# Kernel optimization log

Hardware: AMD Instinct MI355X
Metric: run time of the kernel (lower is better)

## Reference

```python
import jax, jax.numpy as jnp
import numpy as np

TEMP = 0.07
W_MLM, W_LINE, W_QUAT, W_SONNET = 0.5, 0.2, 0.2, 0.1
IGNORE = -100


def setup_inputs() -> dict:
    key = jax.random.key(0)
    ks = jax.random.split(key, 10)
    B, S, V, D = 16, 256, 30522, 768
    P_LINE, N_LINE = 224, 224
    P_QUAT, N_QUAT = 64, 64
    mlm_logits = jax.random.normal(ks[0], (B, S, V), dtype=jnp.float32)
    raw_labels = jax.random.randint(ks[1], (B, S), 0, V)
    mask_prob = jax.random.uniform(ks[2], (B, S))
    mlm_labels = jnp.where(mask_prob < 0.15, raw_labels, IGNORE).astype(jnp.int64)
    return {
        "mlm_logits": mlm_logits,
        "mlm_labels": mlm_labels,
        "line_anchor": jax.random.normal(ks[3], (P_LINE, D), dtype=jnp.float32),
        "line_positive": jax.random.normal(ks[4], (P_LINE, D), dtype=jnp.float32),
        "line_negative": jax.random.normal(ks[5], (N_LINE, D), dtype=jnp.float32),
        "quat_anchor": jax.random.normal(ks[6], (P_QUAT, D), dtype=jnp.float32),
        "quat_positive": jax.random.normal(ks[7], (P_QUAT, D), dtype=jnp.float32),
        "quat_negative": jax.random.normal(ks[8], (N_QUAT, D), dtype=jnp.float32),
        "sonnet_embeddings": jax.random.normal(ks[9], (B, D), dtype=jnp.float32),
    }


def _l2norm(x, eps=1e-12):
    # matches F.normalize(dim=-1)
    n = jnp.sqrt(jnp.sum(x * x, axis=-1, keepdims=True))
    return x / jnp.maximum(n, eps)


def _mlm_loss(logits, labels):
    # cross entropy with ignore_index=-100, mean over valid tokens
    V = logits.shape[-1]
    logits2 = logits.reshape(-1, V)
    labels1 = labels.reshape(-1)
    valid = labels1 != IGNORE
    safe = jnp.where(valid, labels1, 0)
    logp = jax.nn.log_softmax(logits2, axis=-1)
    nll = -jnp.take_along_axis(logp, safe[:, None], axis=-1)[:, 0]
    nll = jnp.where(valid, nll, 0.0)
    return jnp.sum(nll) / jnp.maximum(jnp.sum(valid), 1)


def _infonce(anchor, positive, negatives):
    # batched form of the python-loop pairwise InfoNCE:
    # each anchor scored against its positive and ALL negatives
    a = _l2norm(anchor)                       # [P, D]
    p = _l2norm(positive)                     # [P, D]
    n = _l2norm(negatives)                    # [N, D]
    pos_sim = jnp.sum(a * p, axis=-1) / TEMP  # [P]
    neg_sim = jnp.einsum("pd,nd->pn", a, n) / TEMP  # [P, N]
    logits = jnp.concatenate([pos_sim[:, None], neg_sim], axis=1)  # [P, 1+N]
    loss = jax.nn.logsumexp(logits, axis=1) - pos_sim
    return jnp.mean(loss)


def _sonnet_loss(emb):
    sn = _l2norm(emb)                                  # [B, D]
    sim = jnp.einsum("id,jd->ij", sn, sn) / TEMP       # [B, B]
    diag = jnp.diagonal(sim)
    loss = jax.nn.logsumexp(sim, axis=1) - diag
    return jnp.mean(loss)


def reference(mlm_logits, mlm_labels, line_anchor, line_positive, line_negative,
              quat_anchor, quat_positive, quat_negative, sonnet_embeddings):
    mlm = _mlm_loss(mlm_logits, mlm_labels)
    line = _infonce(line_anchor, line_positive, line_negative)
    quat = _infonce(quat_anchor, quat_positive, quat_negative)
    sonnet = _sonnet_loss(sonnet_embeddings)
    total = W_MLM * mlm + W_LINE * line + W_QUAT * quat + W_SONNET * sonnet
    return total
```

## Files before the change

### kernel.cpp

```cpp
#include <hip/hip_runtime.h>
#include <math.h>
#include <stdint.h>

#define TI (1.0f / 0.07f)
#define VD 768
#define VD4 192
#define VV 30522
#define NROWS 4096
#define P_LINE 224
#define N_LINE 224
#define P_QUAT 64
#define N_QUAT 64

#define WS_NLL   0
#define WS_FLAG  4096
#define WS_LINE  8192
#define WS_QUAT  8416

__device__ __forceinline__ float wave_sum(float v) {
    #pragma unroll
    for (int o = 32; o; o >>= 1) v += __shfl_xor(v, o);
    return v;
}

__global__ __launch_bounds__(256) void mega_kernel(
    const float* __restrict__ logits, const int* __restrict__ labels,
    const float* __restrict__ la, const float* __restrict__ lp, const float* __restrict__ ln_,
    const float* __restrict__ qa, const float* __restrict__ qp, const float* __restrict__ qn,
    float* __restrict__ wsf)
{
    __shared__ float4 sA4[VD4];
    __shared__ float  sred[4][3];

    int b    = blockIdx.x;
    int tid  = threadIdx.x;
    int lane = tid & 63, wave = tid >> 6;

    if (b < NROWS) {
        int lab = labels[b];
        if (lab < 0) {
            if (tid == 0) { wsf[WS_NLL + b] = 0.0f; wsf[WS_FLAG + b] = 0.0f; }
            return;
        }
        const float* row = logits + (size_t)b * VV;
        float xl = (tid == 0) ? row[lab] : 0.0f;

        float s0 = 0.f, s1 = 0.f, s2 = 0.f, s3 = 0.f;
        uintptr_t addr = (uintptr_t)row;
        int head = (int)(((16u - (unsigned)(addr & 15u)) & 15u) >> 2);
        if (tid < head) s0 += __expf(row[tid]);
        int nvec = (VV - head) >> 2;
        const float4* vp = (const float4*)(row + head);
        for (int i = tid; i < nvec; i += 256) {
            float4 v = vp[i];
            s0 += __expf(v.x); s1 += __expf(v.y);
            s2 += __expf(v.z); s3 += __expf(v.w);
        }
        int tail = head + 4 * nvec;
        for (int i = tail + tid; i < VV; i += 256) s0 += __expf(row[i]);

        float s = (s0 + s1) + (s2 + s3);
        s = wave_sum(s);
        if (lane == 0) sred[wave][0] = s;
        __syncthreads();
        if (tid == 0) {
            float S = sred[0][0] + sred[1][0] + sred[2][0] + sred[3][0];
            wsf[WS_NLL + b]  = logf(S) - xl;
            wsf[WS_FLAG + b] = 1.0f;
        }
        return;
    }

    const float *A, *P, *N; int Nn, p; float* lossOut;
    if (b < NROWS + P_LINE) { p = b - NROWS;          A = la; P = lp; N = ln_; Nn = N_LINE; lossOut = wsf + WS_LINE; }
    else                    { p = b - NROWS - P_LINE; A = qa; P = qp; N = qn;  Nn = N_QUAT; lossOut = wsf + WS_QUAT; }

    const float4* A4 = (const float4*)(A + (size_t)p * VD);
    const float4* P4 = (const float4*)(P + (size_t)p * VD);

    float aa = 0.f, ap = 0.f, pp = 0.f;
    if (tid < VD4) {
        float4 a = A4[tid], q = P4[tid];
        sA4[tid] = a;
        aa = a.x*a.x + a.y*a.y + a.z*a.z + a.w*a.w;
        ap = a.x*q.x + a.y*q.y + a.z*q.z + a.w*q.w;
        pp = q.x*q.x + q.y*q.y + q.z*q.z + q.w*q.w;
    }
    aa = wave_sum(aa); ap = wave_sum(ap); pp = wave_sum(pp);
    if (lane == 0) { sred[wave][0] = aa; sred[wave][1] = ap; sred[wave][2] = pp; }
    __syncthreads();
    float taa = sred[0][0] + sred[1][0] + sred[2][0] + sred[3][0];
    float tap = sred[0][1] + sred[1][1] + sred[2][1] + sred[3][1];
    float tpp = sred[0][2] + sred[1][2] + sred[2][2] + sred[3][2];
    float ia  = 1.0f / fmaxf(sqrtf(taa), 1e-12f);
    float ipn = 1.0f / fmaxf(sqrtf(tpp), 1e-12f);
    float pos = tap * ia * ipn * TI;

    float ss = 0.0f;
    for (int n = wave; n < Nn; n += 4) {
        const float4* N4 = (const float4*)(N + (size_t)n * VD);
        float d = 0.f, nn = 0.f;
        #pragma unroll
        for (int k = 0; k < 3; k++) {
            float4 x = N4[lane + 64 * k];
            float4 a = sA4[lane + 64 * k];
            d  += a.x*x.x + a.y*x.y + a.z*x.z + a.w*x.w;
            nn += x.x*x.x + x.y*x.y + x.z*x.z + x.w*x.w;
        }
        #pragma unroll
        for (int o = 32; o; o >>= 1) { d += __shfl_xor(d, o); nn += __shfl_xor(nn, o); }
        float in_ = 1.0f / fmaxf(sqrtf(nn), 1e-12f);
        ss += __expf(d * ia * in_ * TI);
    }
    __syncthreads();
    if (lane == 0) sred[wave][0] = ss;
    __syncthreads();
    if (tid == 0) {
        float S = sred[0][0] + sred[1][0] + sred[2][0] + sred[3][0] + __expf(pos);
        lossOut[p] = logf(S) - pos;
    }
}

__global__ __launch_bounds__(256) void sonnet_combine_kernel(const float* __restrict__ emb,
                                                             const float* __restrict__ wsf,
                                                             float* __restrict__ out) {
    __shared__ float sE[16 * VD];
    __shared__ float sInv[16];
    __shared__ float sSim[16][16];
    __shared__ float sLoss[16];
    __shared__ float red[4][4];
    int tid = threadIdx.x, lane = tid & 63, wave = tid >> 6;

    for (int i = tid; i < 16 * VD; i += 256) sE[i] = emb[i];
    __syncthreads();

    for (int rr = wave; rr < 16; rr += 4) {
        float ssq = 0.0f;
        #pragma unroll
        for (int k = 0; k < 12; k++) { float x = sE[rr * VD + lane + 64 * k]; ssq += x * x; }
        ssq = wave_sum(ssq);
        if (lane == 0) sInv[rr] = 1.0f / fmaxf(sqrtf(ssq), 1e-12f);
    }
    __syncthreads();

    int i = tid >> 4, j = tid & 15;
    if (j >= i) {
        float d = 0.0f;
        for (int kk = 0; kk < VD; kk++) {
            int k = kk + 48 * j; if (k >= VD) k -= VD;
            d += sE[i * VD + k] * sE[j * VD + k];
        }
        sSim[i][j] = d * sInv[i] * sInv[j] * TI;
    }
    __syncthreads();
    if (j < i) sSim[i][j] = sSim[j][i];
    __syncthreads();

    if (tid < 16) {
        float m = -INFINITY;
        #pragma unroll
        for (int c = 0; c < 16; c++) m = fmaxf(m, sSim[tid][c]);
        float s = 0.0f;
        #pragma unroll
        for (int c = 0; c < 16; c++) s += __expf(sSim[tid][c] - m);
        sLoss[tid] = (m + logf(s)) - sSim[tid][tid];
    }
    __syncthreads();

    float nll = 0.0f, cnt = 0.0f, lline = 0.0f, lquat = 0.0f;
    for (int r2 = tid; r2 < NROWS; r2 += 256) { nll += wsf[WS_NLL + r2]; cnt += wsf[WS_FLAG + r2]; }
    for (int r2 = tid; r2 < P_LINE; r2 += 256) lline += wsf[WS_LINE + r2];
    for (int r2 = tid; r2 < P_QUAT; r2 += 256) lquat += wsf[WS_QUAT + r2];
    nll = wave_sum(nll); cnt = wave_sum(cnt); lline = wave_sum(lline); lquat = wave_sum(lquat);
    if (lane == 0) { red[wave][0] = nll; red[wave][1] = cnt; red[wave][2] = lline; red[wave][3] = lquat; }
    __syncthreads();
    if (tid == 0) {
        float tn = 0, tc = 0, tl = 0, tq = 0;
        #pragma unroll
        for (int w = 0; w < 4; w++) { tn += red[w][0]; tc += red[w][1]; tl += red[w][2]; tq += red[w][3]; }
        float sonnet = 0.0f;
        #pragma unroll
        for (int r2 = 0; r2 < 16; r2++) sonnet += sLoss[r2];
        sonnet *= (1.0f / 16.0f);
        float mlm = tn / fmaxf(tc, 1.0f);
        out[0] = 0.5f * mlm + 0.2f * (tl / (float)P_LINE) + 0.2f * (tq / (float)P_QUAT) + 0.1f * sonnet;
    }
}

extern "C" void kernel_launch(void* const* d_in, const int* in_sizes, int n_in,
                              void* d_out, int out_size, void* d_ws, size_t ws_size,
                              hipStream_t stream) {
    const float* mlm_logits = (const float*)d_in[0];
    const int*   mlm_labels = (const int*)d_in[1];
    const float* line_a = (const float*)d_in[2];
    const float* line_p = (const float*)d_in[3];
    const float* line_n = (const float*)d_in[4];
    const float* quat_a = (const float*)d_in[5];
    const float* quat_p = (const float*)d_in[6];
    const float* quat_n = (const float*)d_in[7];
    const float* sonnet = (const float*)d_in[8];
    float* wsf = (float*)d_ws;
    float* out = (float*)d_out;

    mega_kernel<<<NROWS + P_LINE + P_QUAT, 256, 0, stream>>>(
        mlm_logits, mlm_labels, line_a, line_p, line_n, quat_a, quat_p, quat_n, wsf);
    sonnet_combine_kernel<<<1, 256, 0, stream>>>(sonnet, wsf, out);
}
```

Measured before the change: 633.2 us.

## Fuse sonnet loss and final combine into main kernel via atomics and last-block reduction

Merges the single-block sonnet/combine kernel into the main grid as an extra block. Per-row partial losses are now accumulated with float atomics instead of being written to a workspace array, and the last block to finish (tracked by an atomic counter) computes the final weighted sum. This removes the second kernel launch and the serial single-block reduction over 4096 entries. In exchange it adds a memset launch, atomic contention on a few addresses, and a sum order that is no longer deterministic.

```diff
diff --git a/kernel.cpp b/kernel.cpp
--- a/kernel.cpp
+++ b/kernel.cpp
@@ -11,11 +11,8 @@
 #define N_LINE 224
 #define P_QUAT 64
 #define N_QUAT 64
-
-#define WS_NLL   0
-#define WS_FLAG  4096
-#define WS_LINE  8192
-#define WS_QUAT  8416
+#define GRID_TOTAL (NROWS + P_LINE + P_QUAT + 1)
+
 
 __device__ __forceinline__ float wave_sum(float v) {
     #pragma unroll
@@ -23,14 +20,17 @@
     return v;
 }
 
-__global__ __launch_bounds__(256) void mega_kernel(
+__global__ __launch_bounds__(256) void fused_kernel(
     const float* __restrict__ logits, const int* __restrict__ labels,
     const float* __restrict__ la, const float* __restrict__ lp, const float* __restrict__ ln_,
     const float* __restrict__ qa, const float* __restrict__ qp, const float* __restrict__ qn,
-    float* __restrict__ wsf)
+    const float* __restrict__ emb,
+    float* __restrict__ acc, float* __restrict__ out)
 {
     __shared__ float4 sA4[VD4];
     __shared__ float  sred[4][3];
+    __shared__ float  sSim[16][17];
+    __shared__ float  sInv[16];
 
     int b    = blockIdx.x;
     int tid  = threadIdx.x;
@@ -38,152 +38,146 @@
 
     if (b < NROWS) {
         int lab = labels[b];
-        if (lab < 0) {
-            if (tid == 0) { wsf[WS_NLL + b] = 0.0f; wsf[WS_FLAG + b] = 0.0f; }
-            return;
-        }
-        const float* row = logits + (size_t)b * VV;
-        float xl = (tid == 0) ? row[lab] : 0.0f;
-
-        float s0 = 0.f, s1 = 0.f, s2 = 0.f, s3 = 0.f;
-        uintptr_t addr = (uintptr_t)row;
-        int head = (int)(((16u - (unsigned)(addr & 15u)) & 15u) >> 2);
-        if (tid < head) s0 += __expf(row[tid]);
-        int nvec = (VV - head) >> 2;
-        const float4* vp = (const float4*)(row + head);
-        for (int i = tid; i < nvec; i += 256) {
-            float4 v = vp[i];
-            s0 += __expf(v.x); s1 += __expf(v.y);
-            s2 += __expf(v.z); s3 += __expf(v.w);
-        }
-        int tail = head + 4 * nvec;
-        for (int i = tail + tid; i < VV; i += 256) s0 += __expf(row[i]);
-
-        float s = (s0 + s1) + (s2 + s3);
-        s = wave_sum(s);
-        if (lane == 0) sred[wave][0] = s;
+        if (lab >= 0) {
+            const float* row = logits + (size_t)b * VV;
+            float xl = (tid == 0) ? row[lab] : 0.0f;
+            float s0 = 0.f, s1 = 0.f, s2 = 0.f, s3 = 0.f;
+            uintptr_t addr = (uintptr_t)row;
+            int head = (int)(((16u - (unsigned)(addr & 15u)) & 15u) >> 2);
+            if (tid < head) s0 += __expf(row[tid]);
+            int nvec = (VV - head) >> 2;
+            const float4* vp = (const float4*)(row + head);
+            for (int i = tid; i < nvec; i += 256) {
+                float4 v = vp[i];
+                s0 += __expf(v.x); s1 += __expf(v.y);
+                s2 += __expf(v.z); s3 += __expf(v.w);
+            }
+            int tail = head + 4 * nvec;
+            for (int i = tail + tid; i < VV; i += 256) s0 += __expf(row[i]);
+            float s = (s0 + s1) + (s2 + s3);
+            s = wave_sum(s);
+            if (lane == 0) sred[wave][0] = s;
+            __syncthreads();
+            if (tid == 0) {
+                float S = sred[0][0] + sred[1][0] + sred[2][0] + sred[3][0];
+                atomicAdd(&acc[0], logf(S) - xl);
+                atomicAdd(&acc[1], 1.0f);
+            }
+        }
+    } else if (b < NROWS + P_LINE + P_QUAT) {
+        const float *A, *P, *N; int Nn, p, slot;
+        if (b < NROWS + P_LINE) { p = b - NROWS;          A = la; P = lp; N = ln_; Nn = N_LINE; slot = 2; }
+        else                    { p = b - NROWS - P_LINE; A = qa; P = qp; N = qn;  Nn = N_QUAT; slot = 3; }
+
+        const float4* A4 = (const float4*)(A + (size_t)p * VD);
+        const float4* P4 = (const float4*)(P + (size_t)p * VD);
+
+        float aa = 0.f, ap = 0.f, pp = 0.f;
+        if (tid < VD4) {
+            float4 a = A4[tid], q = P4[tid];
+            sA4[tid] = a;
+            aa = a.x*a.x + a.y*a.y + a.z*a.z + a.w*a.w;
+            ap = a.x*q.x + a.y*q.y + a.z*q.z + a.w*q.w;
+            pp = q.x*q.x + q.y*q.y + q.z*q.z + q.w*q.w;
+        }
+        aa = wave_sum(aa); ap = wave_sum(ap); pp = wave_sum(pp);
+        if (lane == 0) { sred[wave][0] = aa; sred[wave][1] = ap; sred[wave][2] = pp; }
+        __syncthreads();
+        float taa = sred[0][0] + sred[1][0] + sred[2][0] + sred[3][0];
+        float tap = sred[0][1] + sred[1][1] + sred[2][1] + sred[3][1];
+        float tpp = sred[0][2] + sred[1][2] + sred[2][2] + sred[3][2];
+        float ia  = 1.0f / fmaxf(sqrtf(taa), 1e-12f);
+        float ipn = 1.0f / fmaxf(sqrtf(tpp), 1e-12f);
+        float pos = tap * ia * ipn * TI;
+
+        float ss = 0.0f;
+        for (int n = wave; n < Nn; n += 4) {
+            const float4* N4 = (const float4*)(N + (size_t)n * VD);
+            float d = 0.f, nn = 0.f;
+            #pragma unroll
+            for (int k = 0; k < 3; k++) {
+                float4 x = N4[lane + 64 * k];
+                float4 a = sA4[lane + 64 * k];
+                d  += a.x*x.x + a.y*x.y + a.z*x.z + a.w*x.w;
+                nn += x.x*x.x + x.y*x.y + x.z*x.z + x.w*x.w;
+            }
+            #pragma unroll
+            for (int o = 32; o; o >>= 1) { d += __shfl_xor(d, o); nn += __shfl_xor(nn, o); }
+            float in_ = 1.0f / fmaxf(sqrtf(nn), 1e-12f);
+            ss += __expf(d * ia * in_ * TI);
+        }
+        __syncthreads();
+        if (lane == 0) sred[wave][0] = ss;
         __syncthreads();
         if (tid == 0) {
-            float S = sred[0][0] + sred[1][0] + sred[2][0] + sred[3][0];
-            wsf[WS_NLL + b]  = logf(S) - xl;
-            wsf[WS_FLAG + b] = 1.0f;
-        }
-        return;
+            float S = sred[0][0] + sred[1][0] + sred[2][0] + sred[3][0] + __expf(pos);
+            atomicAdd(&acc[slot], logf(S) - pos);
+        }
+    } else {
+        for (int rr = wave; rr < 16; rr += 4) {
+            const float4* R = (const float4*)(emb + (size_t)rr * VD);
+            float ssq = 0.f;
+            #pragma unroll
+            for (int k = 0; k < 3; k++) {
+                float4 x = R[lane + 64 * k];
+                ssq += x.x*x.x + x.y*x.y + x.z*x.z + x.w*x.w;
+            }
+            ssq = wave_sum(ssq);
+            if (lane == 0) sInv[rr] = 1.0f / fmaxf(sqrtf(ssq), 1e-12f);
+        }
+        __syncthreads();
+        int q = 0;
+        for (int i = 0; i < 16; i++) {
+            for (int j = i; j < 16; j++, q++) {
+                if ((q & 3) != wave) continue;
+                const float4* Ri = (const float4*)(emb + (size_t)i * VD);
+                const float4* Rj = (const float4*)(emb + (size_t)j * VD);
+                float d = 0.f;
+                #pragma unroll
+                for (int k = 0; k < 3; k++) {
+                    float4 a = Ri[lane + 64 * k];
+                    float4 x = Rj[lane + 64 * k];
+                    d += a.x*x.x + a.y*x.y + a.z*x.z + a.w*x.w;
+                }
+                d = wave_sum(d);
+                if (lane == 0) {
+                    float v = d * sInv[i] * sInv[j] * TI;
+                    sSim[i][j] = v; sSim[j][i] = v;
+                }
+            }
+        }
+        __syncthreads();
+        if (wave == 0) {
+            float l = 0.0f;
+            if (lane < 16) {
+                float m = -INFINITY;
+                #pragma unroll
+                for (int c = 0; c < 16; c++) m = fmaxf(m, sSim[lane][c]);
+                float s2 = 0.f;
+                #pragma unroll
+                for (int c = 0; c < 16; c++) s2 += __expf(sSim[lane][c] - m);
+                l = (m + logf(s2)) - sSim[lane][lane];
+            }
+            l = wave_sum(l);
+            if (lane == 0) atomicAdd(&acc[4], l * (1.0f / 16.0f));
+        }
     }
 
-    const float *A, *P, *N; int Nn, p; float* lossOut;
-    if (b < NROWS + P_LINE) { p = b - NROWS;          A = la; P = lp; N = ln_; Nn = N_LINE; lossOut = wsf + WS_LINE; }
-    else                    { p = b - NROWS - P_LINE; A = qa; P = qp; N = qn;  Nn = N_QUAT; lossOut = wsf + WS_QUAT; }
-
-    const float4* A4 = (const float4*)(A + (size_t)p * VD);
-    const float4* P4 = (const float4*)(P + (size_t)p * VD);
-
-    float aa = 0.f, ap = 0.f, pp = 0.f;
-    if (tid < VD4) {
-        float4 a = A4[tid], q = P4[tid];
-        sA4[tid] = a;
-        aa = a.x*a.x + a.y*a.y + a.z*a.z + a.w*a.w;
-        ap = a.x*q.x + a.y*q.y + a.z*q.z + a.w*q.w;
-        pp = q.x*q.x + q.y*q.y + q.z*q.z + q.w*q.w;
-    }
-    aa = wave_sum(aa); ap = wave_sum(ap); pp = wave_sum(pp);
-    if (lane == 0) { sred[wave][0] = aa; sred[wave][1] = ap; sred[wave][2] = pp; }
-    __syncthreads();
-    float taa = sred[0][0] + sred[1][0] + sred[2][0] + sred[3][0];
-    float tap = sred[0][1] + sred[1][1] + sred[2][1] + sred[3][1];
-    float tpp = sred[0][2] + sred[1][2] + sred[2][2] + sred[3][2];
-    float ia  = 1.0f / fmaxf(sqrtf(taa), 1e-12f);
-    float ipn = 1.0f / fmaxf(sqrtf(tpp), 1e-12f);
-    float pos = tap * ia * ipn * TI;
-
-    float ss = 0.0f;
-    for (int n = wave; n < Nn; n += 4) {
-        const float4* N4 = (const float4*)(N + (size_t)n * VD);
-        float d = 0.f, nn = 0.f;
-        #pragma unroll
-        for (int k = 0; k < 3; k++) {
-            float4 x = N4[lane + 64 * k];
-            float4 a = sA4[lane + 64 * k];
-            d  += a.x*x.x + a.y*x.y + a.z*x.z + a.w*x.w;
-            nn += x.x*x.x + x.y*x.y + x.z*x.z + x.w*x.w;
-        }
-        #pragma unroll
-        for (int o = 32; o; o >>= 1) { d += __shfl_xor(d, o); nn += __shfl_xor(nn, o); }
-        float in_ = 1.0f / fmaxf(sqrtf(nn), 1e-12f);
-        ss += __expf(d * ia * in_ * TI);
-    }
-    __syncthreads();
-    if (lane == 0) sred[wave][0] = ss;
-    __syncthreads();
     if (tid == 0) {
-        float S = sred[0][0] + sred[1][0] + sred[2][0] + sred[3][0] + __expf(pos);
-        lossOut[p] = logf(S) - pos;
-    }
-}
-
-__global__ __launch_bounds__(256) void sonnet_combine_kernel(const float* __restrict__ emb,
-                                                             const float* __restrict__ wsf,
-                                                             float* __restrict__ out) {
-    __shared__ float sE[16 * VD];
-    __shared__ float sInv[16];
-    __shared__ float sSim[16][16];
-    __shared__ float sLoss[16];
-    __shared__ float red[4][4];
-    int tid = threadIdx.x, lane = tid & 63, wave = tid >> 6;
-
-    for (int i = tid; i < 16 * VD; i += 256) sE[i] = emb[i];
-    __syncthreads();
-
-    for (int rr = wave; rr < 16; rr += 4) {
-        float ssq = 0.0f;
-        #pragma unroll
-        for (int k = 0; k < 12; k++) { float x = sE[rr * VD + lane + 64 * k]; ssq += x * x; }
-        ssq = wave_sum(ssq);
-        if (lane == 0) sInv[rr] = 1.0f / fmaxf(sqrtf(ssq), 1e-12f);
-    }
-    __syncthreads();
-
-    int i = tid >> 4, j = tid & 15;
-    if (j >= i) {
-        float d = 0.0f;
-        for (int kk = 0; kk < VD; kk++) {
-            int k = kk + 48 * j; if (k >= VD) k -= VD;
-            d += sE[i * VD + k] * sE[j * VD + k];
-        }
-        sSim[i][j] = d * sInv[i] * sInv[j] * TI;
-    }
-    __syncthreads();
-    if (j < i) sSim[i][j] = sSim[j][i];
-    __syncthreads();
-
-    if (tid < 16) {
-        float m = -INFINITY;
-        #pragma unroll
-        for (int c = 0; c < 16; c++) m = fmaxf(m, sSim[tid][c]);
-        float s = 0.0f;
-        #pragma unroll
-        for (int c = 0; c < 16; c++) s += __expf(sSim[tid][c] - m);
-        sLoss[tid] = (m + logf(s)) - sSim[tid][tid];
-    }
-    __syncthreads();
-
-    float nll = 0.0f, cnt = 0.0f, lline = 0.0f, lquat = 0.0f;
-    for (int r2 = tid; r2 < NROWS; r2 += 256) { nll += wsf[WS_NLL + r2]; cnt += wsf[WS_FLAG + r2]; }
-    for (int r2 = tid; r2 < P_LINE; r2 += 256) lline += wsf[WS_LINE + r2];
-    for (int r2 = tid; r2 < P_QUAT; r2 += 256) lquat += wsf[WS_QUAT + r2];
-    nll = wave_sum(nll); cnt = wave_sum(cnt); lline = wave_sum(lline); lquat = wave_sum(lquat);
-    if (lane == 0) { red[wave][0] = nll; red[wave][1] = cnt; red[wave][2] = lline; red[wave][3] = lquat; }
-    __syncthreads();
-    if (tid == 0) {
-        float tn = 0, tc = 0, tl = 0, tq = 0;
-        #pragma unroll
-        for (int w = 0; w < 4; w++) { tn += red[w][0]; tc += red[w][1]; tl += red[w][2]; tq += red[w][3]; }
-        float sonnet = 0.0f;
-        #pragma unroll
-        for (int r2 = 0; r2 < 16; r2++) sonnet += sLoss[r2];
-        sonnet *= (1.0f / 16.0f);
-        float mlm = tn / fmaxf(tc, 1.0f);
-        out[0] = 0.5f * mlm + 0.2f * (tl / (float)P_LINE) + 0.2f * (tq / (float)P_QUAT) + 0.1f * sonnet;
+        __threadfence();
+        unsigned old = atomicAdd((unsigned int*)&acc[5], 1u);
+        if (old == (unsigned)(GRID_TOTAL - 1)) {
+            __threadfence();
+            float nll = atomicAdd(&acc[0], 0.0f);
+            float cnt = atomicAdd(&acc[1], 0.0f);
+            float tl  = atomicAdd(&acc[2], 0.0f);
+            float tq  = atomicAdd(&acc[3], 0.0f);
+            float sn  = atomicAdd(&acc[4], 0.0f);
+            out[0] = 0.5f * (nll / fmaxf(cnt, 1.0f))
+                   + 0.2f * (tl * (1.0f / (float)P_LINE))
+                   + 0.2f * (tq * (1.0f / (float)P_QUAT))
+                   + 0.1f * sn;
+        }
     }
 }
 
@@ -199,10 +193,11 @@
     const float* quat_p = (const float*)d_in[6];
     const float* quat_n = (const float*)d_in[7];
     const float* sonnet = (const float*)d_in[8];
-    float* wsf = (float*)d_ws;
+    float* acc = (float*)d_ws;
     float* out = (float*)d_out;
 
-    mega_kernel<<<NROWS + P_LINE + P_QUAT, 256, 0, stream>>>(
-        mlm_logits, mlm_labels, line_a, line_p, line_n, quat_a, quat_p, quat_n, wsf);
-    sonnet_combine_kernel<<<1, 256, 0, stream>>>(sonnet, wsf, out);
+    hipMemsetAsync(d_ws, 0, 6 * sizeof(float), stream);
+    fused_kernel<<<GRID_TOTAL, 256, 0, stream>>>(
+        mlm_logits, mlm_labels, line_a, line_p, line_n,
+        quat_a, quat_p, quat_n, sonnet, acc, out);
 }
```

Measured after the change: 698.9 us. 10.4% more time.
